# Optimization experiments

Hardware: AMD Instinct MI355X
Metric: run time of the kernel (lower is better)

The kernel has to match this reference:

```python
import jax, jax.numpy as jnp
import numpy as np

H = 1024
F = 3584
E = 8
TOP_K = 2
B, S = 2, 1024


def setup_inputs() -> dict:
    key = jax.random.key(0)
    ks = jax.random.split(key, 5)
    scale_h = 1.0 / np.sqrt(H)
    scale_f = 1.0 / np.sqrt(F)
    return {
        "hidden_states": jax.random.normal(ks[0], (B, S, H), dtype=jnp.float32),
        "gate_w": jax.random.normal(ks[1], (H, E), dtype=jnp.float32) * scale_h,
        "w1": jax.random.normal(ks[2], (E, H, F), dtype=jnp.float32) * scale_h,
        "w3": jax.random.normal(ks[3], (E, H, F), dtype=jnp.float32) * scale_h,
        "w2": jax.random.normal(ks[4], (E, F, H), dtype=jnp.float32) * scale_f,
        "top_k": TOP_K,
    }


def reference(hidden_states, gate_w, w1, w3, w2, top_k):
    b, s, h = hidden_states.shape
    e = gate_w.shape[1]
    x = hidden_states.reshape(-1, h)  # [N, H]

    # Router: softmax over experts, top-k selection, renormalize (Mixtral).
    logits = x @ gate_w                             # [N, E]
    probs = jax.nn.softmax(logits, axis=-1)
    rw, sel = jax.lax.top_k(probs, top_k)           # [N, K]
    rw = rw / jnp.sum(rw, axis=-1, keepdims=True)

    # Dispatch/combine weights: combine[n, e] = sum_k rw[n,k] * (sel[n,k]==e).
    # This is the mathematical equivalent of moe_permute + weighted moe_unpermute.
    combine = jnp.sum(jax.nn.one_hot(sel, e, dtype=rw.dtype) * rw[..., None], axis=1)  # [N, E]

    # Grouped SwiGLU expert MLPs; loop over the small fixed expert count so the
    # [N, F] intermediate is materialized one expert at a time.
    out = jnp.zeros_like(x)
    for ei in range(e):
        hdn = jax.nn.silu(x @ w1[ei]) * (x @ w3[ei])  # [N, F]
        out = out + combine[:, ei:ei + 1] * (hdn @ w2[ei])
    return out.reshape(b, s, h)
```

## Files before the change

### kernel.cpp

```cpp
#include <hip/hip_runtime.h>
#include <hip/hip_bf16.h>

#define NTOK 2048
#define HD   1024
#define FD   3584
#define NE   8

#define BM 128
#define BN1 64
#define BM2 64
#define BN 128
#define BK 64
#define NIT1 (HD / BK)
#define KS2 2
#define KLEN2 (FD / KS2)
#define NIT2 (KLEN2 / BK)

typedef __attribute__((ext_vector_type(8))) short short8;
typedef __attribute__((ext_vector_type(4))) float f32x4;

__device__ __forceinline__ unsigned short f2bf(float f) {
    __hip_bfloat16 h = __float2bfloat16(f);
    union { __hip_bfloat16 h; unsigned short u; } c; c.h = h;
    return c.u;
}

typedef __attribute__((address_space(1))) const unsigned int g_cu32;
typedef __attribute__((address_space(3))) unsigned int l_u32;
__device__ __forceinline__ void gl16(const void* g, void* l) {
    __builtin_amdgcn_global_load_lds((g_cu32*)g, (l_u32*)(unsigned int)(size_t)l, 16, 0, 0);
}

__global__ void k_router(const float* __restrict__ x, const float* __restrict__ gw,
                         int* __restrict__ sel, float* __restrict__ selw,
                         int* __restrict__ counts) {
    int token = blockIdx.x * 4 + (threadIdx.x >> 6);
    int lane  = threadIdx.x & 63;
    if (token >= NTOK) return;
    const float* xr = x + (size_t)token * HD;
    float acc[NE];
#pragma unroll
    for (int e = 0; e < NE; e++) acc[e] = 0.f;
    for (int h = lane; h < HD; h += 64) {
        float xv = xr[h];
        const float4* g = (const float4*)(gw + (size_t)h * NE);
        float4 g0 = g[0], g1 = g[1];
        acc[0] += xv * g0.x; acc[1] += xv * g0.y; acc[2] += xv * g0.z; acc[3] += xv * g0.w;
        acc[4] += xv * g1.x; acc[5] += xv * g1.y; acc[6] += xv * g1.z; acc[7] += xv * g1.w;
    }
#pragma unroll
    for (int e = 0; e < NE; e++) {
#pragma unroll
        for (int off = 32; off >= 1; off >>= 1) acc[e] += __shfl_xor(acc[e], off, 64);
    }
    if (lane == 0) {
        float m = acc[0];
#pragma unroll
        for (int e = 1; e < NE; e++) m = fmaxf(m, acc[e]);
        float z[NE];
#pragma unroll
        for (int e = 0; e < NE; e++) z[e] = expf(acc[e] - m);
        int e0 = 0; float z0 = z[0];
#pragma unroll
        for (int e = 1; e < NE; e++) if (z[e] > z0) { z0 = z[e]; e0 = e; }
        int e1 = -1; float z1 = -1.f;
#pragma unroll
        for (int e = 0; e < NE; e++) if (e != e0 && z[e] > z1) { z1 = z[e]; e1 = e; }
        float s = z0 + z1;
        sel[token * 2 + 0] = e0; sel[token * 2 + 1] = e1;
        selw[token * 2 + 0] = z0 / s; selw[token * 2 + 1] = z1 / s;
        atomicAdd(&counts[e0], 1);
        atomicAdd(&counts[e1], 1);
    }
}

__global__ void k_scan(const int* __restrict__ counts, int* __restrict__ basep,
                       int* __restrict__ fillc) {
    if (threadIdx.x == 0 && blockIdx.x == 0) {
        int b = 0;
        for (int e = 0; e < NE; e++) { basep[e] = b; b += counts[e]; fillc[e] = 0; }
    }
}

__global__ void k_fill(const int* __restrict__ sel, const float* __restrict__ selw,
                       const int* __restrict__ basep, int* __restrict__ fillc,
                       int* __restrict__ rowmap, int* __restrict__ rowk,
                       float* __restrict__ roww) {
    int n = blockIdx.x * blockDim.x + threadIdx.x;
    if (n >= NTOK) return;
#pragma unroll
    for (int k = 0; k < 2; k++) {
        int e = sel[n * 2 + k];
        int p = atomicAdd(&fillc[e], 1);
        int g = basep[e] + p;
        rowmap[g] = n; rowk[g] = k; roww[g] = selw[n * 2 + k];
    }
}

__global__ void k_cvt(const float* __restrict__ x, unsigned short* __restrict__ xb) {
    size_t i = ((size_t)blockIdx.x * blockDim.x + threadIdx.x) * 8;
    float4 a = *(const float4*)(x + i);
    float4 b = *(const float4*)(x + i + 4);
    unsigned short p[8] __attribute__((aligned(16))) =
        { f2bf(a.x), f2bf(a.y), f2bf(a.z), f2bf(a.w),
          f2bf(b.x), f2bf(b.y), f2bf(b.z), f2bf(b.w) };
    *(uint4*)(xb + i) = *(uint4*)p;
}

__global__ void k_wt3(const float* __restrict__ w1, const float* __restrict__ w3,
                      const float* __restrict__ w2,
                      unsigned short* __restrict__ w1t, unsigned short* __restrict__ w3t,
                      unsigned short* __restrict__ w2t) {
    __shared__ unsigned int P[64 * 32];
    const int z = blockIdx.z;
    int K, N, tx, ty;
    const float* src;
    unsigned short* dst;
    if (z < 16) {
        K = HD; N = FD;
        const int e = z & 7;
        src = (z < 8 ? w1 : w3) + (size_t)e * K * N;
        dst = (z < 8 ? w1t : w3t) + (size_t)e * N * K;
        tx = blockIdx.x % (FD / 64); ty = blockIdx.x / (FD / 64);
    } else {
        K = FD; N = HD;
        const int e = z - 16;
        src = w2 + (size_t)e * K * N;
        dst = w2t + (size_t)e * N * K;
        tx = blockIdx.x % (HD / 64); ty = blockIdx.x / (HD / 64);
    }
    src += (size_t)(ty * 64) * N + tx * 64;
    dst += (size_t)(tx * 64) * K + ty * 64;

    const int t = threadIdx.x;
    {
        const int rp = t >> 3;
        const int c8 = t & 7;
        const float* s0 = src + (size_t)(2 * rp) * N + c8 * 8;
        const float* s1 = s0 + N;
        float4 a0 = *(const float4*)(s0);
        float4 a1 = *(const float4*)(s0 + 4);
        float4 b0 = *(const float4*)(s1);
        float4 b1 = *(const float4*)(s1 + 4);
        float ev[8] = { a0.x, a0.y, a0.z, a0.w, a1.x, a1.y, a1.z, a1.w };
        float od[8] = { b0.x, b0.y, b0.z, b0.w, b1.x, b1.y, b1.z, b1.w };
#pragma unroll
        for (int j = 0; j < 8; j++) {
            const int n = c8 * 8 + j;
            unsigned int v = (unsigned int)f2bf(ev[j]) | ((unsigned int)f2bf(od[j]) << 16);
            P[n * 32 + (rp ^ ((n >> 3) << 2))] = v;
        }
    }
    __syncthreads();
    {
        const int n = t >> 2;
#pragma unroll
        for (int it = 0; it < 2; it++) {
            const int q = (t & 3) + 4 * it;
            uint4 v = *(const uint4*)&P[n * 32 + 4 * (q ^ (n >> 3))];
            *(uint4*)&dst[(size_t)n * K + q * 8] = v;
        }
    }
}

__global__ __launch_bounds__(256, 2) void k_gemm1(
    const unsigned short* __restrict__ xb,
    const unsigned short* __restrict__ w1t, const unsigned short* __restrict__ w3t,
    const int* __restrict__ counts, const int* __restrict__ basep,
    const int* __restrict__ rowmap, unsigned short* __restrict__ act)
{
    const int e = blockIdx.z;
    const int nrows = counts[e];
    const int m0 = blockIdx.y * BM;
    if (m0 >= nrows) return;
    const int f0 = blockIdx.x * BN1;
    const int gbase = basep[e];

    __shared__ __align__(16) unsigned short At[2][BM][BK];
    __shared__ __align__(16) unsigned short B1[2][BN1][BK];
    __shared__ __align__(16) unsigned short B3[2][BN1][BK];

    const int t = threadIdx.x;
    const int lane = t & 63;
    const int w = t >> 6;
    const int wrm = w >> 1, wnn = w & 1;
    const int lr = lane >> 3;
    const int so = ((lane & 7) ^ lr) * 8;

    const unsigned short* asrc[4];
#pragma unroll
    for (int c = 0; c < 4; c++) {
        const int row = (w * 4 + c) * 8 + lr;
        const int tok = rowmap[gbase + min(m0 + row, nrows - 1)];
        asrc[c] = xb + (size_t)tok * HD + so;
    }
    const unsigned short* b1src[2];
    const unsigned short* b3src[2];
#pragma unroll
    for (int c = 0; c < 2; c++) {
        const int row = (w * 2 + c) * 8 + lr;
        b1src[c] = w1t + ((size_t)(e * FD + f0 + row)) * HD + so;
        b3src[c] = w3t + ((size_t)(e * FD + f0 + row)) * HD + so;
    }

    f32x4 acc1[4][2], acc3[4][2];
#pragma unroll
    for (int i = 0; i < 4; i++)
#pragma unroll
        for (int j = 0; j < 2; j++) { acc1[i][j] = (f32x4)(0.f); acc3[i][j] = (f32x4)(0.f); }

    const int l15 = lane & 15;
    const int lhi = lane >> 4;
    const int rs = (l15 & 7) * 8;

#pragma unroll
    for (int c = 0; c < 4; c++) gl16(asrc[c], &At[0][(w * 4 + c) * 8][0]);
#pragma unroll
    for (int c = 0; c < 2; c++) {
        gl16(b1src[c], &B1[0][(w * 2 + c) * 8][0]);
        gl16(b3src[c], &B3[0][(w * 2 + c) * 8][0]);
    }

    for (int it = 0; it < NIT1; ++it) {
        const int cur = it & 1;
        if (it + 1 < NIT1) {
            const int kn = (it + 1) * BK;
#pragma unroll
            for (int c = 0; c < 4; c++) gl16(asrc[c] + kn, &At[cur ^ 1][(w * 4 + c) * 8][0]);
#pragma unroll
            for (int c = 0; c < 2; c++) {
                gl16(b1src[c] + kn, &B1[cur ^ 1][(w * 2 + c) * 8][0]);
                gl16(b3src[c] + kn, &B3[cur ^ 1][(w * 2 + c) * 8][0]);
            }
            asm volatile("s_waitcnt vmcnt(8)" ::: "memory");
        } else {
            asm volatile("s_waitcnt vmcnt(0)" ::: "memory");
        }
        __builtin_amdgcn_s_barrier();
#pragma unroll
        for (int kk = 0; kk < 2; kk++) {
            const int kc = (kk * 32 + lhi * 8) ^ rs;
            short8 af[4], b1f[2], b3f[2];
#pragma unroll
            for (int i = 0; i < 4; i++)
                af[i] = *(const short8*)&At[cur][wrm * 64 + i * 16 + l15][kc];
#pragma unroll
            for (int j = 0; j < 2; j++) {
                b1f[j] = *(const short8*)&B1[cur][wnn * 32 + j * 16 + l15][kc];
                b3f[j] = *(const short8*)&B3[cur][wnn * 32 + j * 16 + l15][kc];
            }
#pragma unroll
            for (int i = 0; i < 4; i++)
#pragma unroll
                for (int j = 0; j < 2; j++) {
                    acc1[i][j] = __builtin_amdgcn_mfma_f32_16x16x32_bf16(af[i], b1f[j], acc1[i][j], 0, 0, 0);
                    acc3[i][j] = __builtin_amdgcn_mfma_f32_16x16x32_bf16(af[i], b3f[j], acc3[i][j], 0, 0, 0);
                }
        }
        __builtin_amdgcn_s_barrier();
    }

    const int rbase = wrm * 64 + lhi * 4;
    const int cbase = f0 + wnn * 32 + l15;
#pragma unroll
    for (int i = 0; i < 4; i++) {
#pragma unroll
        for (int r = 0; r < 4; r++) {
            const int ml = rbase + i * 16 + r;
            if (m0 + ml < nrows) {
                const size_t rowoff = (size_t)(gbase + m0 + ml) * FD;
#pragma unroll
                for (int j = 0; j < 2; j++) {
                    float y1 = acc1[i][j][r];
                    float y3 = acc3[i][j][r];
                    float sv = (y1 / (1.f + __expf(-y1))) * y3;
                    act[rowoff + cbase + j * 16] = f2bf(sv);
                }
            }
        }
    }
}

__global__ __launch_bounds__(256, 4) void k_gemm2(
    const unsigned short* __restrict__ act,
    const unsigned short* __restrict__ w2t,
    const int* __restrict__ counts, const int* __restrict__ basep,
    const int* __restrict__ rowmap, const int* __restrict__ rowk,
    const float* __restrict__ roww, float* __restrict__ out)
{
    const int z = blockIdx.z;
    const int e = z >> 1, ks = z & 1;
    const int nrows = counts[e];
    const int m0 = blockIdx.y * BM2;
    if (m0 >= nrows) return;
    const int h0 = blockIdx.x * BN;
    const int gbase = basep[e];
    const int kbase = ks * KLEN2;

    __shared__ __align__(16) unsigned short At[2][BM2][BK];
    __shared__ __align__(16) unsigned short Bt[2][BN][BK];

    const int t = threadIdx.x;
    const int lane = t & 63;
    const int w = t >> 6;
    const int wr2 = w >> 1, wn2 = w & 1;
    const int lr = lane >> 3;
    const int so = ((lane & 7) ^ lr) * 8;

    const unsigned short* asrc[2];
#pragma unroll
    for (int c = 0; c < 2; c++) {
        const int row = (w * 2 + c) * 8 + lr;
        asrc[c] = act + ((size_t)gbase + min(m0 + row, nrows - 1)) * FD + so + kbase;
    }
    const unsigned short* bsrc[4];
#pragma unroll
    for (int c = 0; c < 4; c++) {
        const int row = (w * 4 + c) * 8 + lr;
        bsrc[c] = w2t + ((size_t)(e * HD + h0 + row)) * FD + so + kbase;
    }

    f32x4 acc[2][4];
#pragma unroll
    for (int i = 0; i < 2; i++)
#pragma unroll
        for (int j = 0; j < 4; j++) acc[i][j] = (f32x4)(0.f);

    const int l15 = lane & 15;
    const int lhi = lane >> 4;
    const int rs = (l15 & 7) * 8;

#pragma unroll
    for (int c = 0; c < 2; c++) gl16(asrc[c], &At[0][(w * 2 + c) * 8][0]);
#pragma unroll
    for (int c = 0; c < 4; c++) gl16(bsrc[c], &Bt[0][(w * 4 + c) * 8][0]);

    for (int it = 0; it < NIT2; ++it) {
        const int cur = it & 1;
        if (it + 1 < NIT2) {
            const int kn = (it + 1) * BK;
#pragma unroll
            for (int c = 0; c < 2; c++) gl16(asrc[c] + kn, &At[cur ^ 1][(w * 2 + c) * 8][0]);
#pragma unroll
            for (int c = 0; c < 4; c++) gl16(bsrc[c] + kn, &Bt[cur ^ 1][(w * 4 + c) * 8][0]);
            asm volatile("s_waitcnt vmcnt(6)" ::: "memory");
        } else {
            asm volatile("s_waitcnt vmcnt(0)" ::: "memory");
        }
        __builtin_amdgcn_s_barrier();
#pragma unroll
        for (int kk = 0; kk < 2; kk++) {
            const int kc = (kk * 32 + lhi * 8) ^ rs;
            short8 af[2], bf[4];
#pragma unroll
            for (int i = 0; i < 2; i++)
                af[i] = *(const short8*)&At[cur][wr2 * 32 + i * 16 + l15][kc];
#pragma unroll
            for (int j = 0; j < 4; j++)
                bf[j] = *(const short8*)&Bt[cur][wn2 * 64 + j * 16 + l15][kc];
#pragma unroll
            for (int i = 0; i < 2; i++)
#pragma unroll
                for (int j = 0; j < 4; j++)
                    acc[i][j] = __builtin_amdgcn_mfma_f32_16x16x32_bf16(af[i], bf[j], acc[i][j], 0, 0, 0);
        }
        __builtin_amdgcn_s_barrier();
    }

    const int rbase = wr2 * 32 + lhi * 4;
    const int cbase = h0 + wn2 * 64 + l15;
#pragma unroll
    for (int i = 0; i < 2; i++) {
#pragma unroll
        for (int r = 0; r < 4; r++) {
            const int ml = rbase + i * 16 + r;
            if (m0 + ml < nrows) {
                const int grow = gbase + m0 + ml;
                const int tok = rowmap[grow];
                const float wv = roww[grow];
                float* op = out + (size_t)tok * HD + cbase;
#pragma unroll
                for (int j = 0; j < 4; j++)
                    atomicAdd(&op[j * 16], acc[i][j][r] * wv);
            }
        }
    }
}

extern "C" void kernel_launch(void* const* d_in, const int* in_sizes, int n_in,
                              void* d_out, int out_size, void* d_ws, size_t ws_size,
                              hipStream_t stream) {
    const float* x  = (const float*)d_in[0];
    const float* gw = (const float*)d_in[1];
    const float* w1 = (const float*)d_in[2];
    const float* w3 = (const float*)d_in[3];
    const float* w2 = (const float*)d_in[4];
    float* out = (float*)d_out;

    char* ws = (char*)d_ws;
    size_t off = 0;
    auto alloc = [&](size_t b) { char* p = ws + off; off += (b + 255) & ~(size_t)255; return p; };
    int*   sel    = (int*)  alloc((size_t)NTOK * 2 * 4);
    float* selw   = (float*)alloc((size_t)NTOK * 2 * 4);
    int*   counts = (int*)  alloc(NE * 4);
    int*   basep  = (int*)  alloc(NE * 4);
    int*   fillc  = (int*)  alloc(NE * 4);
    int*   rowmap = (int*)  alloc((size_t)NTOK * 2 * 4);
    int*   rowk   = (int*)  alloc((size_t)NTOK * 2 * 4);
    float* roww   = (float*)alloc((size_t)NTOK * 2 * 4);
    unsigned short* xb  = (unsigned short*)alloc((size_t)NTOK * HD * 2);
    unsigned short* act = (unsigned short*)alloc((size_t)NTOK * 2 * FD * 2);
    unsigned short* w1t = (unsigned short*)alloc((size_t)NE * HD * FD * 2);
    unsigned short* w3t = (unsigned short*)alloc((size_t)NE * HD * FD * 2);
    unsigned short* w2t = (unsigned short*)alloc((size_t)NE * HD * FD * 2);

    hipMemsetAsync(counts, 0, NE * 4, stream);
    hipMemsetAsync(out, 0, (size_t)out_size * 4, stream);
    k_wt3<<<dim3(896, 1, 24), 256, 0, stream>>>(w1, w3, w2, w1t, w3t, w2t);
    k_cvt<<<(NTOK * HD) / (256 * 8), 256, 0, stream>>>(x, xb);
    k_router<<<NTOK / 4, 256, 0, stream>>>(x, gw, sel, selw, counts);
    k_scan<<<1, 64, 0, stream>>>(counts, basep, fillc);
    k_fill<<<NTOK / 256, 256, 0, stream>>>(sel, selw, basep, fillc, rowmap, rowk, roww);
    k_gemm1<<<dim3(FD / BN1, NTOK / BM, NE), 256, 0, stream>>>(xb, w1t, w3t, counts, basep, rowmap, act);
    k_gemm2<<<dim3(HD / BN, NTOK / BM2, NE * KS2), 256, 0, stream>>>(act, w2t, counts, basep, rowmap, rowk, roww, out);
}
```

Before: 330.5 us.

## Store transposed bf16 expert weights as contiguous 64x64 tiles

The weight-transpose kernel now writes each 64x64 bf16 tile contiguously (4096 elements) instead of in row-major transposed order. Both GEMM kernels compute B-operand addresses from tile indices, so each K-step's weight tile is one contiguous 8KB block rather than 64 rows strided by the full K dimension. This aims to improve DRAM/TLB locality and coalescing for weight streaming, which dominates traffic. It also relies on ks and the tile index math matching the block layout.

```diff
diff --git a/kernel.cpp b/kernel.cpp
--- a/kernel.cpp
+++ b/kernel.cpp
@@ -15,6 +15,7 @@
 #define KS2 2
 #define KLEN2 (FD / KS2)
 #define NIT2 (KLEN2 / BK)
+#define TSZ 4096
 
 typedef __attribute__((ext_vector_type(8))) short short8;
 typedef __attribute__((ext_vector_type(4))) float f32x4;
@@ -113,24 +114,23 @@
                       unsigned short* __restrict__ w2t) {
     __shared__ unsigned int P[64 * 32];
     const int z = blockIdx.z;
-    int K, N, tx, ty;
+    int N, tx, ty;
     const float* src;
     unsigned short* dst;
     if (z < 16) {
-        K = HD; N = FD;
+        N = FD;
         const int e = z & 7;
-        src = (z < 8 ? w1 : w3) + (size_t)e * K * N;
-        dst = (z < 8 ? w1t : w3t) + (size_t)e * N * K;
         tx = blockIdx.x % (FD / 64); ty = blockIdx.x / (FD / 64);
+        src = (z < 8 ? w1 : w3) + (size_t)e * HD * FD;
+        dst = (z < 8 ? w1t : w3t) + (size_t)e * HD * FD + ((size_t)tx * 16 + ty) * TSZ;
     } else {
-        K = FD; N = HD;
+        N = HD;
         const int e = z - 16;
-        src = w2 + (size_t)e * K * N;
-        dst = w2t + (size_t)e * N * K;
         tx = blockIdx.x % (HD / 64); ty = blockIdx.x / (HD / 64);
+        src = w2 + (size_t)e * FD * HD;
+        dst = w2t + (size_t)e * HD * FD + ((size_t)tx * 56 + ty) * TSZ;
     }
     src += (size_t)(ty * 64) * N + tx * 64;
-    dst += (size_t)(tx * 64) * K + ty * 64;
 
     const int t = threadIdx.x;
     {
@@ -153,12 +153,13 @@
     }
     __syncthreads();
     {
-        const int n = t >> 2;
-#pragma unroll
-        for (int it = 0; it < 2; it++) {
-            const int q = (t & 3) + 4 * it;
+        const int n0 = t >> 3;
+        const int q  = t & 7;
+#pragma unroll
+        for (int p = 0; p < 2; p++) {
+            const int n = n0 + 32 * p;
             uint4 v = *(const uint4*)&P[n * 32 + 4 * (q ^ (n >> 3))];
-            *(uint4*)&dst[(size_t)n * K + q * 8] = v;
+            *(uint4*)&dst[n * 64 + q * 8] = v;
         }
     }
 }
@@ -199,8 +200,9 @@
 #pragma unroll
     for (int c = 0; c < 2; c++) {
         const int row = (w * 2 + c) * 8 + lr;
-        b1src[c] = w1t + ((size_t)(e * FD + f0 + row)) * HD + so;
-        b3src[c] = w3t + ((size_t)(e * FD + f0 + row)) * HD + so;
+        const size_t tb = (size_t)e * HD * FD + ((size_t)blockIdx.x * 16) * TSZ + row * 64 + so;
+        b1src[c] = w1t + tb;
+        b3src[c] = w3t + tb;
     }
 
     f32x4 acc1[4][2], acc3[4][2];
@@ -225,12 +227,13 @@
         const int cur = it & 1;
         if (it + 1 < NIT1) {
             const int kn = (it + 1) * BK;
+            const size_t bt = (size_t)(it + 1) * TSZ;
 #pragma unroll
             for (int c = 0; c < 4; c++) gl16(asrc[c] + kn, &At[cur ^ 1][(w * 4 + c) * 8][0]);
 #pragma unroll
             for (int c = 0; c < 2; c++) {
-                gl16(b1src[c] + kn, &B1[cur ^ 1][(w * 2 + c) * 8][0]);
-                gl16(b3src[c] + kn, &B3[cur ^ 1][(w * 2 + c) * 8][0]);
+                gl16(b1src[c] + bt, &B1[cur ^ 1][(w * 2 + c) * 8][0]);
+                gl16(b3src[c] + bt, &B3[cur ^ 1][(w * 2 + c) * 8][0]);
             }
             asm volatile("s_waitcnt vmcnt(8)" ::: "memory");
         } else {
@@ -317,7 +320,9 @@
 #pragma unroll
     for (int c = 0; c < 4; c++) {
         const int row = (w * 4 + c) * 8 + lr;
-        bsrc[c] = w2t + ((size_t)(e * HD + h0 + row)) * FD + so + kbase;
+        const int ntile = (h0 >> 6) + (row >> 6);
+        bsrc[c] = w2t + (size_t)e * HD * FD + ((size_t)ntile * 56 + ks * 28) * TSZ
+                + (row & 63) * 64 + so;
     }
 
     f32x4 acc[2][4];
@@ -339,10 +344,11 @@
         const int cur = it & 1;
         if (it + 1 < NIT2) {
             const int kn = (it + 1) * BK;
+            const size_t bt = (size_t)(it + 1) * TSZ;
 #pragma unroll
             for (int c = 0; c < 2; c++) gl16(asrc[c] + kn, &At[cur ^ 1][(w * 2 + c) * 8][0]);
 #pragma unroll
-            for (int c = 0; c < 4; c++) gl16(bsrc[c] + kn, &Bt[cur ^ 1][(w * 4 + c) * 8][0]);
+            for (int c = 0; c < 4; c++) gl16(bsrc[c] + bt, &Bt[cur ^ 1][(w * 4 + c) * 8][0]);
             asm volatile("s_waitcnt vmcnt(6)" ::: "memory");
         } else {
             asm volatile("s_waitcnt vmcnt(0)" ::: "memory");
```

Result: no change. 329.6 us (-0.3%).
